# Kernel optimization log

Measured on AMD Instinct MI355X. Metric: run time of the kernel, lower is better.

Reference implementation:

```python
import jax, jax.numpy as jnp
import numpy as np

K = 3          # involution kernel size
GROUPS = 32    # channels == GROUPS * K*K
BN_EPS = 1e-5

def _conv1x1(x, W, b):
    # x: (B,C,H,W), W: (Co,C), b: (Co,)
    return jnp.einsum('bchw,oc->bohw', x, W) + b[None, :, None, None]

def setup_inputs() -> dict:
    key = jax.random.key(0)
    ks = jax.random.split(key, 5)
    C = GROUPS * K * K  # 288
    x = jax.random.normal(ks[0], (8, C, 64, 64), dtype=jnp.float32)
    Wi = jax.random.normal(ks[1], (C, C), dtype=jnp.float32) * 0.05
    bi = jnp.zeros((C,), dtype=jnp.float32)
    gamma = jnp.ones((C,), dtype=jnp.float32)
    beta = jnp.zeros((C,), dtype=jnp.float32)
    Wo = jax.random.normal(ks[2], (C, C), dtype=jnp.float32) * 0.05
    bo = jnp.zeros((C,), dtype=jnp.float32)
    return {"x": x, "Wi": Wi, "bi": bi, "gamma": gamma, "beta": beta, "Wo": Wo, "bo": bo}

def reference(x, Wi, bi, gamma, beta, Wo, bo):
    B, C, H, W = x.shape
    # kernel generation branch (stride=1 -> avgpool is identity)
    tmp = jax.nn.relu(_conv1x1(x, Wi, bi))
    # BatchNorm2d in training mode: batch stats over (N,H,W), biased variance
    mean = jnp.mean(tmp, axis=(0, 2, 3), keepdims=True)
    var = jnp.var(tmp, axis=(0, 2, 3), keepdims=True)
    tmp = (tmp - mean) * jax.lax.rsqrt(var + BN_EPS)
    tmp = tmp * gamma[None, :, None, None] + beta[None, :, None, None]
    ker = _conv1x1(tmp, Wo, bo)                       # (B, G*K^2, H, W)
    ker = ker.reshape(B, GROUPS, K * K, H, W)         # (B, G, K^2, H, W)
    # unfold: extract KxK patches with padding (K-1)//2, stride 1
    p = (K - 1) // 2
    xp = jnp.pad(x, ((0, 0), (0, 0), (p, p), (p, p)))
    patches = jnp.stack(
        [xp[:, :, i:i + H, j:j + W] for i in range(K) for j in range(K)],
        axis=2,
    )  # (B, C, K^2, H, W), kernel-position minor — matches torch unfold layout
    patches = patches.reshape(B, GROUPS, C // GROUPS, K * K, H, W)
    # per-pixel dynamic kernel multiply + sum over kernel positions
    out = jnp.einsum('bgkhw,bgckhw->bgchw', ker, patches)
    return out.reshape(B, C, H, W)
```

## Files before the change

kernel.cpp:

```cpp
#include <hip/hip_runtime.h>

#define CH   288
#define GRPS 32
#define CPG  9
#define IMH  64
#define IMW  64
#define HW   4096
#define NB   8
#define NPX  (NB * HW)
#define BN_EPS 1e-5f
#define NSLOT 64

typedef short bf16x8 __attribute__((ext_vector_type(8)));
typedef float f32x4  __attribute__((ext_vector_type(4)));

#define XT_OFF   0u
#define WIB_OFF  18874368u
#define WOS_OFF  19040256u
#define SC_OFF   19208448u
#define SH_OFF   19209600u
#define BO2_OFF  19210752u

#define BUF1 20480
#define BUF2 22528

__device__ __forceinline__ unsigned short f2b(float f) {
    unsigned int u = __float_as_uint(f);
    return (unsigned short)((u + 0x7fffu + ((u >> 16) & 1u)) >> 16);
}
__device__ __forceinline__ float b2f(unsigned short h) {
    return __uint_as_float(((unsigned int)h) << 16);
}

#define GLDS(g, l) __builtin_amdgcn_global_load_lds( \
    (const __attribute__((address_space(1))) void*)(g), \
    (__attribute__((address_space(3))) void*)(l), 16, 0, 0)

__device__ __forceinline__ f32x4 mfma16(bf16x8 a, bf16x8 b, f32x4 c) {
    return __builtin_amdgcn_mfma_f32_16x16x32_bf16(a, b, c, 0, 0, 0);
}

#define TS 40
__global__ __launch_bounds__(256) void k_transpose(const float* __restrict__ x,
                                                   unsigned short* __restrict__ xt) {
    __shared__ unsigned short T[64 * TS];
    const int tid = threadIdx.x;
    const int p0 = blockIdx.x * 64;
    const int c0 = blockIdx.y * 32;
    const int b  = blockIdx.z;
    #pragma unroll
    for (int it = 0; it < 2; ++it) {
        const int item  = it * 256 + tid;
        const int c_loc = item >> 4;
        const int p4    = item & 15;
        const float4 v = *(const float4*)(x + (size_t)(b * CH + c0 + c_loc) * HW + p0 + p4 * 4);
        const int px = p4 * 4;
        T[(px + 0) * TS + c_loc] = f2b(v.x);
        T[(px + 1) * TS + c_loc] = f2b(v.y);
        T[(px + 2) * TS + c_loc] = f2b(v.z);
        T[(px + 3) * TS + c_loc] = f2b(v.w);
    }
    __syncthreads();
    const int px_loc = tid >> 2;
    const int cq     = tid & 3;
    const uint4 o = *(const uint4*)((const char*)T + px_loc * (TS * 2) + cq * 16);
    *(uint4*)(xt + ((size_t)b * HW + p0 + px_loc) * CH + c0 + cq * 8) = o;
}

__global__ __launch_bounds__(256) void k_cvt_wi(const float* __restrict__ Wi,
                                                unsigned short* __restrict__ Wib) {
    const int idx = blockIdx.x * 256 + threadIdx.x;
    const float4 v = ((const float4*)Wi)[idx];
    unsigned short h[4] = {f2b(v.x), f2b(v.y), f2b(v.z), f2b(v.w)};
    *(uint2*)(Wib + (size_t)idx * 4) = *(const uint2*)h;
}

__global__ __launch_bounds__(256, 4) void k_gemm1(const unsigned short* __restrict__ Wib,
                                                  const float* __restrict__ bi,
                                                  unsigned short* __restrict__ xt,
                                                  float* __restrict__ slots) {
    __shared__ char smc[2 * BUF1];

    const int tid  = threadIdx.x;
    const int wave = tid >> 6;
    const int lane = tid & 63;
    const int q    = lane >> 4;
    const int r    = lane & 15;
    const int pxh  = wave & 1;
    const int chh  = wave >> 1;
    const int p0   = blockIdx.x * 32;
    const int lrow = lane >> 2;
    const int lp   = lane & 3;

    f32x4 acc[9];
    #pragma unroll
    for (int j = 0; j < 9; ++j) acc[j] = (f32x4)0.0f;

    const unsigned short* xsrc = xt + (size_t)p0 * CH;

    #define STAGE1(K0v, DST) do {                                              \
        for (int s = wave; s < 20; s += 4) {                                   \
            const int row = s * 16 + lrow;                                     \
            const int sc  = lp ^ ((row >> 1) & 3);                             \
            const unsigned short* g = (s < 2)                                  \
                ? xsrc + (size_t)row * CH + (K0v) + sc * 8                     \
                : Wib  + (size_t)(row - 32) * CH + (K0v) + sc * 8;             \
            GLDS(g, (DST) + s * 1024);                                         \
        }                                                                      \
    } while (0)

    #define GSTEP1(BUF) do {                                                   \
        const int xr = pxh * 16 + r;                                           \
        const bf16x8 xf = *(const bf16x8*)((BUF) + xr * 64 +                   \
                             ((q ^ ((xr >> 1) & 3)) * 16));                    \
        _Pragma("unroll")                                                      \
        for (int j = 0; j < 9; ++j) {                                          \
            const int wr = 32 + chh * 144 + j * 16 + r;                        \
            const bf16x8 wf = *(const bf16x8*)((BUF) + wr * 64 +               \
                                 ((q ^ ((wr >> 1) & 3)) * 16));                \
            acc[j] = mfma16(wf, xf, acc[j]);                                   \
        }                                                                      \
    } while (0)

    STAGE1(0, smc);
    asm volatile("s_waitcnt vmcnt(0)" ::: "memory");
    __builtin_amdgcn_s_barrier();
    #pragma unroll 1
    for (int kk = 0; kk < 8; ++kk) {
        STAGE1((kk + 1) * 32, smc + ((kk + 1) & 1) * BUF1);
        asm volatile("s_waitcnt vmcnt(5)" ::: "memory");
        __builtin_amdgcn_s_barrier();
        GSTEP1(smc + (kk & 1) * BUF1);
        __builtin_amdgcn_s_barrier();
    }
    asm volatile("s_waitcnt vmcnt(0)" ::: "memory");
    __builtin_amdgcn_s_barrier();
    GSTEP1(smc);
    __syncthreads();

    float* sstat = (float*)(smc + 38656);
    for (int c2 = tid; c2 < 576; c2 += 256) sstat[c2] = 0.0f;
    __syncthreads();

    #pragma unroll 1
    for (int j = 0; j < 9; ++j) {
        const int cb = chh * 144 + j * 16 + q * 4;
        const float4 b4 = *(const float4*)(bi + cb);
        float v[4];
        v[0] = fmaxf(acc[j][0] + b4.x, 0.0f);
        v[1] = fmaxf(acc[j][1] + b4.y, 0.0f);
        v[2] = fmaxf(acc[j][2] + b4.z, 0.0f);
        v[3] = fmaxf(acc[j][3] + b4.w, 0.0f);
        unsigned short h[4] = {f2b(v[0]), f2b(v[1]), f2b(v[2]), f2b(v[3])};
        *(uint2*)(smc + (pxh * 16 + r) * 576 + cb * 2) = *(const uint2*)h;
        float a1[4] = {v[0], v[1], v[2], v[3]};
        float a2[4] = {v[0]*v[0], v[1]*v[1], v[2]*v[2], v[3]*v[3]};
        #pragma unroll
        for (int m = 1; m < 16; m <<= 1) {
            #pragma unroll
            for (int i = 0; i < 4; ++i) {
                a1[i] += __shfl_xor(a1[i], m, 64);
                a2[i] += __shfl_xor(a2[i], m, 64);
            }
        }
        if (r == 0) {
            #pragma unroll
            for (int i = 0; i < 4; ++i) {
                atomicAdd(&sstat[cb + i], a1[i]);
                atomicAdd(&sstat[288 + cb + i], a2[i]);
            }
        }
    }
    __syncthreads();

    for (int idx = tid; idx < 1152; idx += 256) {
        const int row = idx / 36;
        const int off = idx - row * 36;
        *(uint4*)(xt + (size_t)(p0 + row) * CH + off * 8) =
            *(const uint4*)(smc + row * 576 + off * 16);
    }
    float* slot = slots + (size_t)(blockIdx.x & (NSLOT - 1)) * 576;
    for (int c2 = tid; c2 < 576; c2 += 256)
        atomicAdd(&slot[c2], sstat[c2]);
}

__global__ __launch_bounds__(576) void k_scale(const float* __restrict__ slots,
                                               const float* __restrict__ gamma,
                                               const float* __restrict__ beta,
                                               float* __restrict__ scale,
                                               float* __restrict__ shift) {
    __shared__ float red[576];
    const int tid = threadIdx.x;
    float s = 0.0f;
    #pragma unroll 4
    for (int sl = 0; sl < NSLOT; ++sl) s += slots[sl * 576 + tid];
    red[tid] = s;
    __syncthreads();
    if (tid < CH) {
        const float inv  = 1.0f / (float)(NB * HW);
        const float mean = red[tid] * inv;
        const float var  = red[288 + tid] * inv - mean * mean;
        const float rs   = rsqrtf(var + BN_EPS);
        const float sc   = gamma[tid] * rs;
        scale[tid] = sc;
        shift[tid] = beta[tid] - mean * sc;
    }
}

__global__ __launch_bounds__(64) void k_fold(const float* __restrict__ Wo,
                                             const float* __restrict__ bo,
                                             const float* __restrict__ scale,
                                             const float* __restrict__ shift,
                                             unsigned short* __restrict__ Wos,
                                             float* __restrict__ bo2) {
    const int m = blockIdx.x;
    const int t = threadIdx.x;
    float s = 0.0f;
    for (int k = t; k < CH; k += 64) {
        const float wv = Wo[(size_t)m * CH + k];
        s += wv * shift[k];
        Wos[(size_t)m * CH + k] = f2b(wv * scale[k]);
    }
    #pragma unroll
    for (int off = 32; off > 0; off >>= 1) s += __shfl_down(s, off, 64);
    if (t == 0) bo2[m] = bo[m] + s;
}

#define KLS2 68
__global__ __launch_bounds__(256) void k_gemm2_invol(const unsigned short* __restrict__ xt,
                                                     const unsigned short* __restrict__ Wos,
                                                     const float* __restrict__ bo2,
                                                     const float* __restrict__ x,
                                                     float* __restrict__ out) {
    __shared__ char smc[2 * BUF2];
    unsigned short* kerL = (unsigned short*)smc;

    const int tid  = threadIdx.x;
    const int wave = tid >> 6;
    const int lane = tid & 63;
    const int q    = lane >> 4;
    const int r    = lane & 15;
    const int pxh  = wave & 1;
    const int chh  = wave >> 1;
    const int p0   = blockIdx.x * 64;
    const int b    = blockIdx.y;
    const int h    = blockIdx.x;
    const size_t rowbase = (size_t)b * HW + p0;
    const int lrow = lane >> 2;
    const int lp   = lane & 3;

    f32x4 acc[2][9];
    #pragma unroll
    for (int t = 0; t < 2; ++t)
        #pragma unroll
        for (int j = 0; j < 9; ++j) acc[t][j] = (f32x4)0.0f;

    const unsigned short* xsrc = xt + rowbase * CH;

    #define STAGE2(K0v, DST) do {                                              \
        for (int s = wave; s < 22; s += 4) {                                   \
            const int row = s * 16 + lrow;                                     \
            const int sc  = lp ^ ((row >> 1) & 3);                             \
            const unsigned short* g = (s < 4)                                  \
                ? xsrc + (size_t)row * CH + (K0v) + sc * 8                     \
                : Wos  + (size_t)(row - 64) * CH + (K0v) + sc * 8;             \
            GLDS(g, (DST) + s * 1024);                                         \
        }                                                                      \
    } while (0)

    #define GSTEP2(BUF) do {                                                   \
        bf16x8 xf0, xf1;                                                       \
        { const int xr = pxh * 32 + r;                                         \
          xf0 = *(const bf16x8*)((BUF) + xr * 64 +                             \
                     ((q ^ ((xr >> 1) & 3)) * 16)); }                          \
        { const int xr = pxh * 32 + 16 + r;                                    \
          xf1 = *(const bf16x8*)((BUF) + xr * 64 +                             \
                     ((q ^ ((xr >> 1) & 3)) * 16)); }                          \
        _Pragma("unroll")                                                      \
        for (int j = 0; j < 9; ++j) {                                          \
            const int wr = 64 + chh * 144 + j * 16 + r;                        \
            const bf16x8 wf = *(const bf16x8*)((BUF) + wr * 64 +               \
                                 ((q ^ ((wr >> 1) & 3)) * 16));                \
            acc[0][j] = mfma16(wf, xf0, acc[0][j]);                            \
            acc[1][j] = mfma16(wf, xf1, acc[1][j]);                            \
        }                                                                      \
    } while (0)

    STAGE2(0, smc);
    asm volatile("s_waitcnt vmcnt(0)" ::: "memory");
    __builtin_amdgcn_s_barrier();
    #pragma unroll 1
    for (int kk = 0; kk < 8; ++kk) {
        STAGE2((kk + 1) * 32, smc + ((kk + 1) & 1) * BUF2);
        if (wave < 2) { asm volatile("s_waitcnt vmcnt(6)" ::: "memory"); }
        else          { asm volatile("s_waitcnt vmcnt(5)" ::: "memory"); }
        __builtin_amdgcn_s_barrier();
        GSTEP2(smc + (kk & 1) * BUF2);
        __builtin_amdgcn_s_barrier();
    }
    asm volatile("s_waitcnt vmcnt(0)" ::: "memory");
    __builtin_amdgcn_s_barrier();
    GSTEP2(smc);
    __syncthreads();

    #pragma unroll
    for (int j = 0; j < 9; ++j) {
        const int cb = chh * 144 + j * 16 + q * 4;
        const float4 bz = *(const float4*)(bo2 + cb);
        #pragma unroll
        for (int t = 0; t < 2; ++t) {
            const int pxl = pxh * 32 + t * 16 + r;
            kerL[(cb + 0) * KLS2 + pxl] = f2b(acc[t][j][0] + bz.x);
            kerL[(cb + 1) * KLS2 + pxl] = f2b(acc[t][j][1] + bz.y);
            kerL[(cb + 2) * KLS2 + pxl] = f2b(acc[t][j][2] + bz.z);
            kerL[(cb + 3) * KLS2 + pxl] = f2b(acc[t][j][3] + bz.w);
        }
    }
    __syncthreads();

    const int tm = tid >> 4;
    const int tn = tid & 15;
    const int wb = tn * 4;
    #pragma unroll 1
    for (int i = 0; i < 18; ++i) {
        const int ch = tm + 16 * i;
        const int cb = (ch / CPG) * CPG;
        float xv[3][6];
        #pragma unroll
        for (int dr = 0; dr < 3; ++dr) {
            const int hh = h + dr - 1;
            const bool rv = (hh >= 0) && (hh < IMH);
            const float* xr2 = x + ((size_t)(b * CH + ch) * IMH + (rv ? hh : 0)) * IMW;
            if (rv) {
                const float4 m4 = *(const float4*)(xr2 + wb);
                xv[dr][1] = m4.x; xv[dr][2] = m4.y; xv[dr][3] = m4.z; xv[dr][4] = m4.w;
                xv[dr][0] = (wb > 0)       ? xr2[wb - 1] : 0.0f;
                xv[dr][5] = (wb + 4 < IMW) ? xr2[wb + 4] : 0.0f;
            } else {
                #pragma unroll
                for (int j = 0; j < 6; ++j) xv[dr][j] = 0.0f;
            }
        }
        float o[4] = {0.0f, 0.0f, 0.0f, 0.0f};
        #pragma unroll
        for (int k = 0; k < 9; ++k) {
            const int dr = k / 3, dc = k % 3;
            const uint2 kk = *(const uint2*)(kerL + (cb + k) * KLS2 + tn * 4);
            const unsigned short* ks = (const unsigned short*)&kk;
            #pragma unroll
            for (int j = 0; j < 4; ++j)
                o[j] += b2f(ks[j]) * xv[dr][j + dc];
        }
        float4 ov = {o[0], o[1], o[2], o[3]};
        *(float4*)(out + ((size_t)(b * CH + ch) * IMH + h) * IMW + wb) = ov;
    }
}

extern "C" void kernel_launch(void* const* d_in, const int* in_sizes, int n_in,
                              void* d_out, int out_size, void* d_ws, size_t ws_size,
                              hipStream_t stream) {
    const float* x     = (const float*)d_in[0];
    const float* Wi    = (const float*)d_in[1];
    const float* bi    = (const float*)d_in[2];
    const float* gamma = (const float*)d_in[3];
    const float* beta  = (const float*)d_in[4];
    const float* Wo    = (const float*)d_in[5];
    const float* bo    = (const float*)d_in[6];
    float* out = (float*)d_out;

    char* ws = (char*)d_ws;
    unsigned short* xt  = (unsigned short*)(ws + XT_OFF);
    unsigned short* Wib = (unsigned short*)(ws + WIB_OFF);
    unsigned short* Wos = (unsigned short*)(ws + WOS_OFF);
    float* slots = (float*)(ws + WOS_OFF);
    float* scale = (float*)(ws + SC_OFF);
    float* shift = (float*)(ws + SH_OFF);
    float* bo2   = (float*)(ws + BO2_OFF);

    k_transpose<<<dim3(HW / 64, CH / 32, NB), 256, 0, stream>>>(x, xt);
    k_cvt_wi<<<dim3(CH * CH / 1024), 256, 0, stream>>>(Wi, Wib);
    hipMemsetAsync(ws + WOS_OFF, 0, NSLOT * 576 * sizeof(float), stream);
    k_gemm1<<<dim3(NPX / 32), 256, 0, stream>>>(Wib, bi, xt, slots);
    k_scale<<<dim3(1), 576, 0, stream>>>(slots, gamma, beta, scale, shift);
    k_fold<<<dim3(CH), 64, 0, stream>>>(Wo, bo, scale, shift, Wos, bo2);
    k_gemm2_invol<<<dim3(HW / 64, NB), 256, 0, stream>>>(xt, Wos, bo2, x, out);
}
```

Before: 187.9 us.

## Drop transpose kernel, load x fragments directly and use pre-swizzled tiled layouts

Removes the separate x transpose/bf16-convert pass. GEMM1 now reads fp32 x straight from NCHW into per-lane bf16 MFMA fragments held in registers, and only stages weights through LDS. Weights and the intermediate activation are written in a k-tiled, pre-swizzled layout so that every stage becomes a contiguous 1 KB global_load_lds. Scheduling fences are added around the waits and barriers. This saves a full read and write of the activation tensor, but the strided scalar fp32 loads of x in GEMM1 may be poorly coalesced, and the fragments raise register pressure.

```diff
diff --git a/kernel.cpp b/kernel.cpp
--- a/kernel.cpp
+++ b/kernel.cpp
@@ -14,15 +14,13 @@
 typedef short bf16x8 __attribute__((ext_vector_type(8)));
 typedef float f32x4  __attribute__((ext_vector_type(4)));
 
-#define XT_OFF   0u
+#define TT_OFF   0u
 #define WIB_OFF  18874368u
 #define WOS_OFF  19040256u
 #define SC_OFF   19208448u
 #define SH_OFF   19209600u
 #define BO2_OFF  19210752u
 
-#define BUF1 20480
-#define BUF2 22528
 
 __device__ __forceinline__ unsigned short f2b(float f) {
     unsigned int u = __float_as_uint(f);
@@ -36,50 +34,35 @@
     (const __attribute__((address_space(1))) void*)(g), \
     (__attribute__((address_space(3))) void*)(l), 16, 0, 0)
 
+#define SFENCE __builtin_amdgcn_sched_barrier(0)
+
 __device__ __forceinline__ f32x4 mfma16(bf16x8 a, bf16x8 b, f32x4 c) {
     return __builtin_amdgcn_mfma_f32_16x16x32_bf16(a, b, c, 0, 0, 0);
 }
 
-#define TS 40
-__global__ __launch_bounds__(256) void k_transpose(const float* __restrict__ x,
-                                                   unsigned short* __restrict__ xt) {
-    __shared__ unsigned short T[64 * TS];
-    const int tid = threadIdx.x;
-    const int p0 = blockIdx.x * 64;
-    const int c0 = blockIdx.y * 32;
-    const int b  = blockIdx.z;
-    #pragma unroll
-    for (int it = 0; it < 2; ++it) {
-        const int item  = it * 256 + tid;
-        const int c_loc = item >> 4;
-        const int p4    = item & 15;
-        const float4 v = *(const float4*)(x + (size_t)(b * CH + c0 + c_loc) * HW + p0 + p4 * 4);
-        const int px = p4 * 4;
-        T[(px + 0) * TS + c_loc] = f2b(v.x);
-        T[(px + 1) * TS + c_loc] = f2b(v.y);
-        T[(px + 2) * TS + c_loc] = f2b(v.z);
-        T[(px + 3) * TS + c_loc] = f2b(v.w);
-    }
-    __syncthreads();
-    const int px_loc = tid >> 2;
-    const int cq     = tid & 3;
-    const uint4 o = *(const uint4*)((const char*)T + px_loc * (TS * 2) + cq * 16);
-    *(uint4*)(xt + ((size_t)b * HW + p0 + px_loc) * CH + c0 + cq * 8) = o;
-}
-
 __global__ __launch_bounds__(256) void k_cvt_wi(const float* __restrict__ Wi,
-                                                unsigned short* __restrict__ Wib) {
-    const int idx = blockIdx.x * 256 + threadIdx.x;
-    const float4 v = ((const float4*)Wi)[idx];
-    unsigned short h[4] = {f2b(v.x), f2b(v.y), f2b(v.z), f2b(v.w)};
-    *(uint2*)(Wib + (size_t)idx * 4) = *(const uint2*)h;
-}
-
-__global__ __launch_bounds__(256, 4) void k_gemm1(const unsigned short* __restrict__ Wib,
+                                                unsigned short* __restrict__ WiT) {
+    const int id = blockIdx.x * 256 + threadIdx.x;
+    if (id >= 288 * 36) return;
+    const int row  = id / 36;
+    const int rest = id - row * 36;
+    const int kk   = rest >> 2;
+    const int slot = rest & 3;
+    const int c0   = kk * 32 + ((slot ^ ((row >> 1) & 3)) << 3);
+    const float4 a = *(const float4*)(Wi + (size_t)row * CH + c0);
+    const float4 b = *(const float4*)(Wi + (size_t)row * CH + c0 + 4);
+    unsigned short h[8] = {f2b(a.x), f2b(a.y), f2b(a.z), f2b(a.w),
+                           f2b(b.x), f2b(b.y), f2b(b.z), f2b(b.w)};
+    *(uint4*)(WiT + (size_t)kk * 9216 + row * 32 + slot * 8) = *(const uint4*)h;
+}
+
+#define WSL 18432
+__global__ __launch_bounds__(256, 4) void k_gemm1(const unsigned short* __restrict__ WiT,
                                                   const float* __restrict__ bi,
-                                                  unsigned short* __restrict__ xt,
+                                                  const float* __restrict__ x,
+                                                  unsigned short* __restrict__ tmpT,
                                                   float* __restrict__ slots) {
-    __shared__ char smc[2 * BUF1];
+    __shared__ char smc[2 * WSL];
 
     const int tid  = threadIdx.x;
     const int wave = tid >> 6;
@@ -89,56 +72,67 @@
     const int pxh  = wave & 1;
     const int chh  = wave >> 1;
     const int p0   = blockIdx.x * 32;
-    const int lrow = lane >> 2;
-    const int lp   = lane & 3;
+    const int bidb = p0 >> 12;
+    const int pix  = (p0 & 4095) + pxh * 16 + r;
+
+    bf16x8 frag[9];
+    const float* xs = x + (size_t)(bidb * CH + q * 8) * HW + pix;
+    #pragma unroll
+    for (int kk = 0; kk < 9; ++kk) {
+        unsigned short h[8];
+        #pragma unroll
+        for (int j = 0; j < 8; ++j) h[j] = f2b(xs[(size_t)(kk * 32 + j) * HW]);
+        frag[kk] = *(const bf16x8*)h;
+    }
 
     f32x4 acc[9];
     #pragma unroll
     for (int j = 0; j < 9; ++j) acc[j] = (f32x4)0.0f;
 
-    const unsigned short* xsrc = xt + (size_t)p0 * CH;
-
-    #define STAGE1(K0v, DST) do {                                              \
-        for (int s = wave; s < 20; s += 4) {                                   \
-            const int row = s * 16 + lrow;                                     \
-            const int sc  = lp ^ ((row >> 1) & 3);                             \
-            const unsigned short* g = (s < 2)                                  \
-                ? xsrc + (size_t)row * CH + (K0v) + sc * 8                     \
-                : Wib  + (size_t)(row - 32) * CH + (K0v) + sc * 8;             \
-            GLDS(g, (DST) + s * 1024);                                         \
+    #define STAGE_W1(KK, DST) do {                                             \
+        for (int s = wave; s < 18; s += 4)                                     \
+            GLDS(WiT + (size_t)(KK) * 9216 + s * 512 + lane * 8,               \
+                 (DST) + s * 1024);                                            \
+    } while (0)
+
+    #define GSTEP1(KK, BUF) do {                                               \
+        _Pragma("unroll")                                                      \
+        for (int j = 0; j < 9; ++j) {                                          \
+            const int wr = chh * 144 + j * 16 + r;                             \
+            const bf16x8 wf = *(const bf16x8*)((BUF) + wr * 64 +               \
+                                 ((q ^ ((wr >> 1) & 3)) * 16));                \
+            acc[j] = mfma16(wf, frag[KK], acc[j]);                             \
         }                                                                      \
     } while (0)
 
-    #define GSTEP1(BUF) do {                                                   \
-        const int xr = pxh * 16 + r;                                           \
-        const bf16x8 xf = *(const bf16x8*)((BUF) + xr * 64 +                   \
-                             ((q ^ ((xr >> 1) & 3)) * 16));                    \
-        _Pragma("unroll")                                                      \
-        for (int j = 0; j < 9; ++j) {                                          \
-            const int wr = 32 + chh * 144 + j * 16 + r;                        \
-            const bf16x8 wf = *(const bf16x8*)((BUF) + wr * 64 +               \
-                                 ((q ^ ((wr >> 1) & 3)) * 16));                \
-            acc[j] = mfma16(wf, xf, acc[j]);                                   \
-        }                                                                      \
-    } while (0)
-
-    STAGE1(0, smc);
+    STAGE_W1(0, smc);
+    SFENCE;
     asm volatile("s_waitcnt vmcnt(0)" ::: "memory");
+    SFENCE;
     __builtin_amdgcn_s_barrier();
-    #pragma unroll 1
+    SFENCE;
+    #pragma unroll
     for (int kk = 0; kk < 8; ++kk) {
-        STAGE1((kk + 1) * 32, smc + ((kk + 1) & 1) * BUF1);
-        asm volatile("s_waitcnt vmcnt(5)" ::: "memory");
+        STAGE_W1(kk + 1, smc + ((kk + 1) & 1) * WSL);
+        SFENCE;
+        if (wave < 2) { asm volatile("s_waitcnt vmcnt(5)" ::: "memory"); }
+        else          { asm volatile("s_waitcnt vmcnt(4)" ::: "memory"); }
+        SFENCE;
         __builtin_amdgcn_s_barrier();
-        GSTEP1(smc + (kk & 1) * BUF1);
+        SFENCE;
+        GSTEP1(kk, smc + (kk & 1) * WSL);
+        SFENCE;
         __builtin_amdgcn_s_barrier();
+        SFENCE;
     }
     asm volatile("s_waitcnt vmcnt(0)" ::: "memory");
+    SFENCE;
     __builtin_amdgcn_s_barrier();
-    GSTEP1(smc);
-    __syncthreads();
-
-    float* sstat = (float*)(smc + 38656);
+    SFENCE;
+    GSTEP1(8, smc);
+    __syncthreads();
+
+    float* sstat = (float*)(smc + 34560);
     for (int c2 = tid; c2 < 576; c2 += 256) sstat[c2] = 0.0f;
     __syncthreads();
 
@@ -176,7 +170,10 @@
     for (int idx = tid; idx < 1152; idx += 256) {
         const int row = idx / 36;
         const int off = idx - row * 36;
-        *(uint4*)(xt + (size_t)(p0 + row) * CH + off * 8) =
+        const int kk  = off >> 2;
+        const int p   = off & 3;
+        const int slot = p ^ ((row >> 1) & 3);
+        *(uint4*)(tmpT + (size_t)blockIdx.x * 9216 + kk * 1024 + row * 32 + slot * 8) =
             *(const uint4*)(smc + row * 576 + off * 16);
     }
     float* slot = slots + (size_t)(blockIdx.x & (NSLOT - 1)) * 576;
@@ -211,24 +208,32 @@
                                              const float* __restrict__ bo,
                                              const float* __restrict__ scale,
                                              const float* __restrict__ shift,
-                                             unsigned short* __restrict__ Wos,
+                                             unsigned short* __restrict__ WosT,
                                              float* __restrict__ bo2) {
     const int m = blockIdx.x;
     const int t = threadIdx.x;
     float s = 0.0f;
-    for (int k = t; k < CH; k += 64) {
-        const float wv = Wo[(size_t)m * CH + k];
-        s += wv * shift[k];
-        Wos[(size_t)m * CH + k] = f2b(wv * scale[k]);
-    }
+    for (int k = t; k < CH; k += 64) s += Wo[(size_t)m * CH + k] * shift[k];
     #pragma unroll
     for (int off = 32; off > 0; off >>= 1) s += __shfl_down(s, off, 64);
     if (t == 0) bo2[m] = bo[m] + s;
-}
-
+
+    if (t < 36) {
+        const int kk   = t >> 2;
+        const int slot = t & 3;
+        const int c0   = kk * 32 + ((slot ^ ((m >> 1) & 3)) << 3);
+        unsigned short h[8];
+        #pragma unroll
+        for (int j = 0; j < 8; ++j)
+            h[j] = f2b(Wo[(size_t)m * CH + c0 + j] * scale[c0 + j]);
+        *(uint4*)(WosT + (size_t)kk * 9216 + m * 32 + slot * 8) = *(const uint4*)h;
+    }
+}
+
+#define BUF2 22528
 #define KLS2 68
-__global__ __launch_bounds__(256) void k_gemm2_invol(const unsigned short* __restrict__ xt,
-                                                     const unsigned short* __restrict__ Wos,
+__global__ __launch_bounds__(256) void k_gemm2_invol(const unsigned short* __restrict__ tmpT,
+                                                     const unsigned short* __restrict__ WosT,
                                                      const float* __restrict__ bo2,
                                                      const float* __restrict__ x,
                                                      float* __restrict__ out) {
@@ -242,12 +247,9 @@
     const int r    = lane & 15;
     const int pxh  = wave & 1;
     const int chh  = wave >> 1;
-    const int p0   = blockIdx.x * 64;
     const int b    = blockIdx.y;
     const int h    = blockIdx.x;
-    const size_t rowbase = (size_t)b * HW + p0;
-    const int lrow = lane >> 2;
-    const int lp   = lane & 3;
+    const int P0   = b * 128 + h * 2;
 
     f32x4 acc[2][9];
     #pragma unroll
@@ -255,15 +257,12 @@
         #pragma unroll
         for (int j = 0; j < 9; ++j) acc[t][j] = (f32x4)0.0f;
 
-    const unsigned short* xsrc = xt + rowbase * CH;
-
-    #define STAGE2(K0v, DST) do {                                              \
+    #define STAGE2(KK, DST) do {                                               \
         for (int s = wave; s < 22; s += 4) {                                   \
-            const int row = s * 16 + lrow;                                     \
-            const int sc  = lp ^ ((row >> 1) & 3);                             \
             const unsigned short* g = (s < 4)                                  \
-                ? xsrc + (size_t)row * CH + (K0v) + sc * 8                     \
-                : Wos  + (size_t)(row - 64) * CH + (K0v) + sc * 8;             \
+                ? tmpT + (size_t)(P0 + (s >> 1)) * 9216 + (KK) * 1024          \
+                       + (s & 1) * 512 + lane * 8                              \
+                : WosT + (size_t)(KK) * 9216 + (s - 4) * 512 + lane * 8;       \
             GLDS(g, (DST) + s * 1024);                                         \
         }                                                                      \
     } while (0)
@@ -287,19 +286,29 @@
     } while (0)
 
     STAGE2(0, smc);
+    SFENCE;
     asm volatile("s_waitcnt vmcnt(0)" ::: "memory");
+    SFENCE;
     __builtin_amdgcn_s_barrier();
+    SFENCE;
     #pragma unroll 1
     for (int kk = 0; kk < 8; ++kk) {
-        STAGE2((kk + 1) * 32, smc + ((kk + 1) & 1) * BUF2);
+        STAGE2(kk + 1, smc + ((kk + 1) & 1) * BUF2);
+        SFENCE;
         if (wave < 2) { asm volatile("s_waitcnt vmcnt(6)" ::: "memory"); }
         else          { asm volatile("s_waitcnt vmcnt(5)" ::: "memory"); }
+        SFENCE;
         __builtin_amdgcn_s_barrier();
+        SFENCE;
         GSTEP2(smc + (kk & 1) * BUF2);
+        SFENCE;
         __builtin_amdgcn_s_barrier();
+        SFENCE;
     }
     asm volatile("s_waitcnt vmcnt(0)" ::: "memory");
+    SFENCE;
     __builtin_amdgcn_s_barrier();
+    SFENCE;
     GSTEP2(smc);
     __syncthreads();
 
@@ -369,19 +378,18 @@
     float* out = (float*)d_out;
 
     char* ws = (char*)d_ws;
-    unsigned short* xt  = (unsigned short*)(ws + XT_OFF);
-    unsigned short* Wib = (unsigned short*)(ws + WIB_OFF);
-    unsigned short* Wos = (unsigned short*)(ws + WOS_OFF);
+    unsigned short* tmpT = (unsigned short*)(ws + TT_OFF);
+    unsigned short* WiT  = (unsigned short*)(ws + WIB_OFF);
+    unsigned short* WosT = (unsigned short*)(ws + WOS_OFF);
     float* slots = (float*)(ws + WOS_OFF);
     float* scale = (float*)(ws + SC_OFF);
     float* shift = (float*)(ws + SH_OFF);
     float* bo2   = (float*)(ws + BO2_OFF);
 
-    k_transpose<<<dim3(HW / 64, CH / 32, NB), 256, 0, stream>>>(x, xt);
-    k_cvt_wi<<<dim3(CH * CH / 1024), 256, 0, stream>>>(Wi, Wib);
+    k_cvt_wi<<<dim3(41), 256, 0, stream>>>(Wi, WiT);
     hipMemsetAsync(ws + WOS_OFF, 0, NSLOT * 576 * sizeof(float), stream);
-    k_gemm1<<<dim3(NPX / 32), 256, 0, stream>>>(Wib, bi, xt, slots);
+    k_gemm1<<<dim3(NPX / 32), 256, 0, stream>>>(WiT, bi, x, tmpT, slots);
     k_scale<<<dim3(1), 576, 0, stream>>>(slots, gamma, beta, scale, shift);
-    k_fold<<<dim3(CH), 64, 0, stream>>>(Wo, bo, scale, shift, Wos, bo2);
-    k_gemm2_invol<<<dim3(HW / 64, NB), 256, 0, stream>>>(xt, Wos, bo2, x, out);
-}
+    k_fold<<<dim3(CH), 64, 0, stream>>>(Wo, bo, scale, shift, WosT, bo2);
+    k_gemm2_invol<<<dim3(HW / 64, NB), 256, 0, stream>>>(tmpT, WosT, bo2, x, out);
+}
```

Result: slower. 202.4 us (+7.7%).

## Fuse preprocessing kernels and fold BN finalize into gemm1 last-block tail

Applied to the files above, without the earlier changes.

Merges the input transpose, Wi bf16 conversion and slot zeroing into one pre-kernel. It also removes the separate scale and fold kernels: the last gemm1 block, detected with an atomic counter, reduces the BN slots, computes scale and shift, and writes the folded Wos and bo2. This cuts the launch count from six kernels plus a memset to three, removing launch gaps. In exchange, the BN finalize and weight fold now run serially inside a single workgroup, with uncoalesced per-row loops over Wo.

```diff
diff --git a/kernel.cpp b/kernel.cpp
--- a/kernel.cpp
+++ b/kernel.cpp
@@ -10,6 +10,7 @@
 #define NPX  (NB * HW)
 #define BN_EPS 1e-5f
 #define NSLOT 64
+#define NBLK1 (NPX / 32)
 
 typedef short bf16x8 __attribute__((ext_vector_type(8)));
 typedef float f32x4  __attribute__((ext_vector_type(4)));
@@ -41,13 +42,30 @@
 }
 
 #define TS 40
-__global__ __launch_bounds__(256) void k_transpose(const float* __restrict__ x,
-                                                   unsigned short* __restrict__ xt) {
+__global__ __launch_bounds__(256) void k_pre(const float* __restrict__ x,
+                                             unsigned short* __restrict__ xt,
+                                             const float* __restrict__ Wi,
+                                             unsigned short* __restrict__ Wib,
+                                             float* __restrict__ slots) {
     __shared__ unsigned short T[64 * TS];
     const int tid = threadIdx.x;
     const int p0 = blockIdx.x * 64;
     const int c0 = blockIdx.y * 32;
     const int b  = blockIdx.z;
+
+    if (blockIdx.z == 0) {
+        if (blockIdx.y == 0) {
+            for (int i = blockIdx.x * 256 + tid; i < NSLOT * 576 + 1; i += 64 * 256)
+                slots[i] = 0.0f;
+        } else if (blockIdx.y == 1) {
+            for (int i = blockIdx.x * 256 + tid; i < CH * CH / 4; i += 64 * 256) {
+                const float4 v = ((const float4*)Wi)[i];
+                unsigned short h[4] = {f2b(v.x), f2b(v.y), f2b(v.z), f2b(v.w)};
+                *(uint2*)(Wib + (size_t)i * 4) = *(const uint2*)h;
+            }
+        }
+    }
+
     #pragma unroll
     for (int it = 0; it < 2; ++it) {
         const int item  = it * 256 + tid;
@@ -67,19 +85,18 @@
     *(uint4*)(xt + ((size_t)b * HW + p0 + px_loc) * CH + c0 + cq * 8) = o;
 }
 
-__global__ __launch_bounds__(256) void k_cvt_wi(const float* __restrict__ Wi,
-                                                unsigned short* __restrict__ Wib) {
-    const int idx = blockIdx.x * 256 + threadIdx.x;
-    const float4 v = ((const float4*)Wi)[idx];
-    unsigned short h[4] = {f2b(v.x), f2b(v.y), f2b(v.z), f2b(v.w)};
-    *(uint2*)(Wib + (size_t)idx * 4) = *(const uint2*)h;
-}
-
 __global__ __launch_bounds__(256, 4) void k_gemm1(const unsigned short* __restrict__ Wib,
                                                   const float* __restrict__ bi,
                                                   unsigned short* __restrict__ xt,
-                                                  float* __restrict__ slots) {
+                                                  float* __restrict__ slots,
+                                                  const float* __restrict__ gamma,
+                                                  const float* __restrict__ beta,
+                                                  const float* __restrict__ Wo,
+                                                  const float* __restrict__ bo,
+                                                  unsigned short* __restrict__ Wos,
+                                                  float* __restrict__ bo2) {
     __shared__ char smc[2 * BUF1];
+    __shared__ int lastFlag;
 
     const int tid  = threadIdx.x;
     const int wave = tid >> 6;
@@ -182,48 +199,57 @@
     float* slot = slots + (size_t)(blockIdx.x & (NSLOT - 1)) * 576;
     for (int c2 = tid; c2 < 576; c2 += 256)
         atomicAdd(&slot[c2], sstat[c2]);
-}
-
-__global__ __launch_bounds__(576) void k_scale(const float* __restrict__ slots,
-                                               const float* __restrict__ gamma,
-                                               const float* __restrict__ beta,
-                                               float* __restrict__ scale,
-                                               float* __restrict__ shift) {
-    __shared__ float red[576];
-    const int tid = threadIdx.x;
-    float s = 0.0f;
-    #pragma unroll 4
-    for (int sl = 0; sl < NSLOT; ++sl) s += slots[sl * 576 + tid];
-    red[tid] = s;
-    __syncthreads();
-    if (tid < CH) {
+
+    unsigned int* counter = (unsigned int*)(slots + NSLOT * 576);
+    if (tid == 0) {
+        __threadfence();
+        const unsigned int old = atomicAdd(counter, 1u);
+        lastFlag = (old == (unsigned int)(NBLK1 - 1));
+    }
+    __syncthreads();
+    if (!lastFlag) return;
+    __threadfence();
+
+    float* sumL   = (float*)(smc + 8192);
+    float* scaleL = (float*)(smc);
+    float* shiftL = (float*)(smc + 2048);
+
+    for (int c = tid; c < 576; c += 256) {
+        float s = 0.0f;
+        #pragma unroll 8
+        for (int sl = 0; sl < NSLOT; ++sl)
+            s += atomicAdd(&slots[sl * 576 + c], 0.0f);
+        sumL[c] = s;
+    }
+    __syncthreads();
+    for (int c = tid; c < CH; c += 256) {
         const float inv  = 1.0f / (float)(NB * HW);
-        const float mean = red[tid] * inv;
-        const float var  = red[288 + tid] * inv - mean * mean;
+        const float mean = sumL[c] * inv;
+        const float var  = sumL[288 + c] * inv - mean * mean;
         const float rs   = rsqrtf(var + BN_EPS);
-        const float sc   = gamma[tid] * rs;
-        scale[tid] = sc;
-        shift[tid] = beta[tid] - mean * sc;
-    }
-}
-
-__global__ __launch_bounds__(64) void k_fold(const float* __restrict__ Wo,
-                                             const float* __restrict__ bo,
-                                             const float* __restrict__ scale,
-                                             const float* __restrict__ shift,
-                                             unsigned short* __restrict__ Wos,
-                                             float* __restrict__ bo2) {
-    const int m = blockIdx.x;
-    const int t = threadIdx.x;
-    float s = 0.0f;
-    for (int k = t; k < CH; k += 64) {
-        const float wv = Wo[(size_t)m * CH + k];
-        s += wv * shift[k];
-        Wos[(size_t)m * CH + k] = f2b(wv * scale[k]);
-    }
-    #pragma unroll
-    for (int off = 32; off > 0; off >>= 1) s += __shfl_down(s, off, 64);
-    if (t == 0) bo2[m] = bo[m] + s;
+        const float sc   = gamma[c] * rs;
+        scaleL[c] = sc;
+        shiftL[c] = beta[c] - mean * sc;
+    }
+    __syncthreads();
+    for (int m = tid; m < CH; m += 256) {
+        float s = bo[m];
+        #pragma unroll 8
+        for (int k = 0; k < CH; ++k) s += Wo[(size_t)m * CH + k] * shiftL[k];
+        bo2[m] = s;
+    }
+    for (int id = tid; id < CH * 36; id += 256) {
+        const int m  = id / 36;
+        const int c0 = (id - m * 36) * 8;
+        const float4 a = *(const float4*)(Wo + (size_t)m * CH + c0);
+        const float4 b = *(const float4*)(Wo + (size_t)m * CH + c0 + 4);
+        unsigned short h[8] = {
+            f2b(a.x * scaleL[c0 + 0]), f2b(a.y * scaleL[c0 + 1]),
+            f2b(a.z * scaleL[c0 + 2]), f2b(a.w * scaleL[c0 + 3]),
+            f2b(b.x * scaleL[c0 + 4]), f2b(b.y * scaleL[c0 + 5]),
+            f2b(b.z * scaleL[c0 + 6]), f2b(b.w * scaleL[c0 + 7])};
+        *(uint4*)(Wos + (size_t)m * CH + c0) = *(const uint4*)h;
+    }
 }
 
 #define KLS2 68
@@ -373,15 +399,10 @@
     unsigned short* Wib = (unsigned short*)(ws + WIB_OFF);
     unsigned short* Wos = (unsigned short*)(ws + WOS_OFF);
     float* slots = (float*)(ws + WOS_OFF);
-    float* scale = (float*)(ws + SC_OFF);
-    float* shift = (float*)(ws + SH_OFF);
     float* bo2   = (float*)(ws + BO2_OFF);
 
-    k_transpose<<<dim3(HW / 64, CH / 32, NB), 256, 0, stream>>>(x, xt);
-    k_cvt_wi<<<dim3(CH * CH / 1024), 256, 0, stream>>>(Wi, Wib);
-    hipMemsetAsync(ws + WOS_OFF, 0, NSLOT * 576 * sizeof(float), stream);
-    k_gemm1<<<dim3(NPX / 32), 256, 0, stream>>>(Wib, bi, xt, slots);
-    k_scale<<<dim3(1), 576, 0, stream>>>(slots, gamma, beta, scale, shift);
-    k_fold<<<dim3(CH), 64, 0, stream>>>(Wo, bo, scale, shift, Wos, bo2);
+    k_pre<<<dim3(HW / 64, CH / 32, NB), 256, 0, stream>>>(x, xt, Wi, Wib, slots);
+    k_gemm1<<<dim3(NBLK1), 256, 0, stream>>>(Wib, bi, xt, slots,
+                                             gamma, beta, Wo, bo, Wos, bo2);
     k_gemm2_invol<<<dim3(HW / 64, NB), 256, 0, stream>>>(xt, Wos, bo2, x, out);
 }
```

Result: slower. 242.1 us (+28.8%).
